# Optimization experiments

Hardware: AMD Instinct MI355X
Metric: run time of the kernel (lower is better)

The kernel has to match this reference:

```python
import jax, jax.numpy as jnp
import numpy as np

D_MODEL = 64
N_HEAD = 4
HEAD_DIM = D_MODEL // N_HEAD  # 16


def setup_inputs() -> dict:
    key = jax.random.key(0)
    ks = jax.random.split(key, 8)
    B, T_dec, T_enc = 16, 1024, 1024
    s = 1.0 / np.sqrt(D_MODEL)
    return {
        "x": jax.random.normal(ks[0], (B, T_dec, D_MODEL), dtype=jnp.float32),
        "encoder_outputs": jax.random.normal(ks[1], (B, T_enc, D_MODEL), dtype=jnp.float32),
        "encoder_outputs_mask": jnp.ones((B, T_enc), dtype=jnp.int32),
        "Wkv": jax.random.normal(ks[2], (D_MODEL, 2 * D_MODEL), dtype=jnp.float32) * s,
        "bkv": jnp.zeros((2 * D_MODEL,), dtype=jnp.float32),
        "Wq": jax.random.normal(ks[3], (D_MODEL, D_MODEL), dtype=jnp.float32) * s,
        "bq": jnp.zeros((D_MODEL,), dtype=jnp.float32),
        "Wproj": jax.random.normal(ks[4], (D_MODEL, D_MODEL), dtype=jnp.float32) * s,
        "bproj": jnp.zeros((D_MODEL,), dtype=jnp.float32),
    }


def reference(x, encoder_outputs, encoder_outputs_mask, Wkv, bkv, Wq, bq, Wproj, bproj):
    B, T_dec, C = x.shape
    T_enc = encoder_outputs.shape[1]
    kv = encoder_outputs @ Wkv + bkv                      # [B, T_enc, 2C]
    k, v = kv[..., :D_MODEL], kv[..., D_MODEL:]          # [B, T_enc, C]
    q = x @ Wq + bq                                      # [B, T_dec, C]
    q = q.reshape(B, T_dec, N_HEAD, HEAD_DIM)
    k = k.reshape(B, T_enc, N_HEAD, HEAD_DIM)
    v = v.reshape(B, T_enc, N_HEAD, HEAD_DIM)
    scale = 1.0 / jnp.sqrt(jnp.asarray(HEAD_DIM, dtype=q.dtype))
    att = jnp.einsum("bqhd,bkhd->bhqk", q, k) * scale    # [B, H, T_dec, T_enc]
    mask = (encoder_outputs_mask == 0)[:, None, None, :]  # [B, 1, 1, T_enc]
    att = jnp.where(mask, jnp.asarray(-jnp.inf, dtype=att.dtype), att)
    att = jax.nn.softmax(att, axis=-1)
    ctx = jnp.einsum("bhqk,bkhd->bqhd", att, v).reshape(B, T_dec, C)
    # dropout is identity at eval time
    return ctx @ Wproj + bproj
```

## Files before the change

### kernel.cpp

```cpp
#include <hip/hip_runtime.h>
#include <hip/hip_bf16.h>
#include <math.h>

#define DM 64
#define NH 4
#define HD 16
#define BATCH 16
#define TSEQ 1024

typedef short bf16x8 __attribute__((ext_vector_type(8)));
typedef short bf16x4 __attribute__((ext_vector_type(4)));
typedef float f32x4  __attribute__((ext_vector_type(4)));
typedef float f32x16 __attribute__((ext_vector_type(16)));
typedef unsigned int u32x4 __attribute__((ext_vector_type(4)));

static __device__ inline short f2bf(float x) {
    __hip_bfloat16 h = __float2bfloat16(x);
    return __builtin_bit_cast(short, h);
}
static __device__ inline float bf2f(short s) {
    __hip_bfloat16 h = __builtin_bit_cast(__hip_bfloat16, s);
    return __bfloat162float(h);
}
static __device__ inline unsigned pkbf(float a, float b) {
    unsigned r;
    asm("v_cvt_pk_bf16_f32 %0, %1, %2" : "=v"(r) : "v"(a), "v"(b));
    return r;
}

__global__ __launch_bounds__(256) void proj_kernel(
    const float* __restrict__ x, const float* __restrict__ enc,
    const float* __restrict__ Wkv, const float* __restrict__ bkv,
    const float* __restrict__ Wq,  const float* __restrict__ bq,
    const int* __restrict__ mask,
    short* __restrict__ qhi, short* __restrict__ qlo,
    short* __restrict__ khi, short* __restrict__ klo,
    short* __restrict__ vtt)
{
    const int t = threadIdx.x;
    const int part = blockIdx.y;
    const int r = blockIdx.x * 256 + t;
    const int b = r >> 10, trow = r & 1023;

    const float* in; const float* W; const float* bias; int cb, ldw;
    if (part < 4)      { in = x;   W = Wq;  ldw = 64;  cb = part*16;          bias = bq;  }
    else if (part < 8) { in = enc; W = Wkv; ldw = 128; cb = (part-4)*16;      bias = bkv; }
    else               { in = enc; W = Wkv; ldw = 128; cb = 64 + (part-8)*16; bias = bkv; }

    __shared__ float wsl[64][16];
    for (int idx = t; idx < 1024; idx += 256)
        wsl[idx >> 4][idx & 15] = W[(idx >> 4)*ldw + cb + (idx & 15)];

    float4 xr[16];
    const float4* inrow = (const float4*)(in + (size_t)r * 64);
    #pragma unroll
    for (int i = 0; i < 16; ++i) xr[i] = inrow[i];
    __syncthreads();

    float acc[16];
    #pragma unroll
    for (int j = 0; j < 16; ++j) acc[j] = bias[cb + j];
    #pragma unroll
    for (int k = 0; k < 64; ++k) {
        const float xv = ((const float*)xr)[k];
        const float4 w0 = ((const float4*)&wsl[k][0])[0];
        const float4 w1 = ((const float4*)&wsl[k][0])[1];
        const float4 w2 = ((const float4*)&wsl[k][0])[2];
        const float4 w3 = ((const float4*)&wsl[k][0])[3];
        acc[0]  += xv*w0.x; acc[1]  += xv*w0.y; acc[2]  += xv*w0.z; acc[3]  += xv*w0.w;
        acc[4]  += xv*w1.x; acc[5]  += xv*w1.y; acc[6]  += xv*w1.z; acc[7]  += xv*w1.w;
        acc[8]  += xv*w2.x; acc[9]  += xv*w2.y; acc[10] += xv*w2.z; acc[11] += xv*w2.w;
        acc[12] += xv*w3.x; acc[13] += xv*w3.y; acc[14] += xv*w3.z; acc[15] += xv*w3.w;
    }

    if (part < 8) {
        const float scale = (part < 4) ? 0.36067376022224085f : 1.0f;
        short* dh = (part < 4) ? qhi : khi;
        short* dl = (part < 4) ? qlo : klo;
        const int h = (part < 4) ? part : (part - 4);
        bf16x8 h0, h1, l0, l1;
        #pragma unroll
        for (int j = 0; j < 16; ++j) {
            float vf = acc[j] * scale;
            short hb = f2bf(vf);
            short lb = f2bf(vf - bf2f(hb));
            if (j < 8) { h0[j] = hb; l0[j] = lb; }
            else       { h1[j-8] = hb; l1[j-8] = lb; }
        }
        size_t off = (((size_t)(b*NH + h))*TSEQ + trow)*HD;
        *(bf16x8*)(dh + off)     = h0;
        *(bf16x8*)(dh + off + 8) = h1;
        *(bf16x8*)(dl + off)     = l0;
        *(bf16x8*)(dl + off + 8) = l1;
    } else {
        const int h = part - 8;
        const float mb = (mask[b*TSEQ + trow] != 0) ? 1.0f : 0.0f;
        short* tile = vtt + ((size_t)(b*NH + h))*32768 + (size_t)(trow >> 5)*1024;
        const int kw = trow & 31;
        #pragma unroll
        for (int j = 0; j < 16; ++j)
            tile[j*32 + kw] = f2bf(acc[j] * mb);
        tile[16*32 + kw] = (mb != 0.0f) ? (short)0x3F80 : (short)0;
    }
}

__global__ __launch_bounds__(512) void attn_kernel(
    const short* __restrict__ qhi, const short* __restrict__ qlo,
    const short* __restrict__ khi, const short* __restrict__ klo,
    const short* __restrict__ vtt,
    const float* __restrict__ Wproj, const float* __restrict__ bproj,
    float* __restrict__ out)
{
    const int tid  = threadIdx.x;
    const int lane = tid & 63;
    const int wid  = __builtin_amdgcn_readfirstlane(tid >> 6);
    const int h  = wid & 3;
    const int ks = wid >> 2;
    const int l31 = lane & 31, half = lane >> 5;

    const int bi  = blockIdx.x;
    const int xcd = bi & 7, u = bi >> 3;
    const int b     = xcd + ((u >> 5) << 3);
    const int qbase = (u & 31) * 32;

    __shared__ float Cbuf[2][32][68];
    __shared__ float Lbuf[2][NH][32];
    __shared__ u32x4 Wl[2][4][2][64];

    #pragma unroll
    for (int it = 0; it < 2; ++it) {
        const int s = tid + it*512;
        const int lane6 = s & 63;
        const int hl  = (s >> 6) & 1;
        const int stp = (s >> 7) & 3;
        const int ctc = s >> 9;
        const int c  = ctc*32 + (lane6 & 31);
        const int kb = stp*16 + (lane6 >> 5)*8;
        u32x4 wv;
        #pragma unroll
        for (int jj = 0; jj < 4; ++jj) {
            const float w0 = Wproj[(kb + 2*jj)*DM + c];
            const float w1 = Wproj[(kb + 2*jj + 1)*DM + c];
            if (hl == 0) {
                wv[jj] = pkbf(w0, w1);
            } else {
                const float h0 = bf2f(f2bf(w0));
                const float h1 = bf2f(f2bf(w1));
                wv[jj] = pkbf(w0 - h0, w1 - h1);
            }
        }
        Wl[ctc][stp][hl][lane6] = wv;
    }
    __syncthreads();

    const size_t qoff = (((size_t)(b*NH + h))*TSEQ + qbase + l31)*HD + half*8;
    const bf16x8 qAh = *(const bf16x8*)(qhi + qoff);
    const bf16x8 qAl = *(const bf16x8*)(qlo + qoff);

    const short* khb = khi + (((size_t)(b*NH + h))*TSEQ + ks*512)*HD;
    const short* klb = klo + (((size_t)(b*NH + h))*TSEQ + ks*512)*HD;
    const short* vtb = vtt + ((size_t)(b*NH + h))*32768 + (size_t)ks*16384;

    f32x16 Cacc;
    #pragma unroll
    for (int i = 0; i < 16; ++i) Cacc[i] = 0.f;

    for (int step = 0; step < 16; ++step) {
        const int ko = step * 32;
        const bf16x8 kBh = *(const bf16x8*)(khb + (size_t)(ko + l31)*HD + half*8);
        const bf16x8 kBl = *(const bf16x8*)(klb + (size_t)(ko + l31)*HD + half*8);
        const short* tile = vtb + (size_t)step * 1024;
        const bf16x8 vB0 = *(const bf16x8*)(tile + l31*32 + half*8);
        const bf16x8 vB1 = *(const bf16x8*)(tile + l31*32 + 16 + half*8);

        f32x16 S;
        #pragma unroll
        for (int i = 0; i < 16; ++i) S[i] = 0.f;
        S = __builtin_amdgcn_mfma_f32_32x32x16_bf16(kBh, qAh, S, 0, 0, 0);
        S = __builtin_amdgcn_mfma_f32_32x32x16_bf16(kBl, qAh, S, 0, 0, 0);
        S = __builtin_amdgcn_mfma_f32_32x32x16_bf16(kBh, qAl, S, 0, 0, 0);

        float p[16];
        #pragma unroll
        for (int i = 0; i < 16; ++i) p[i] = __builtin_amdgcn_exp2f(S[i]);

        unsigned a0 = pkbf(p[0],  p[1]),  b0 = pkbf(p[4],  p[5]);
        unsigned a1 = pkbf(p[2],  p[3]),  b1 = pkbf(p[6],  p[7]);
        unsigned a2 = pkbf(p[8],  p[9]),  b2 = pkbf(p[12], p[13]);
        unsigned a3 = pkbf(p[10], p[11]), b3 = pkbf(p[14], p[15]);
        asm("v_permlane32_swap_b32 %0, %1" : "+v"(a0), "+v"(b0));
        asm("v_permlane32_swap_b32 %0, %1" : "+v"(a1), "+v"(b1));
        asm("v_permlane32_swap_b32 %0, %1" : "+v"(a2), "+v"(b2));
        asm("v_permlane32_swap_b32 %0, %1" : "+v"(a3), "+v"(b3));
        u32x4 P0v; P0v[0] = a0; P0v[1] = a1; P0v[2] = b0; P0v[3] = b1;
        u32x4 P1v; P1v[0] = a2; P1v[1] = a3; P1v[2] = b2; P1v[3] = b3;
        const bf16x8 pA0 = __builtin_bit_cast(bf16x8, P0v);
        const bf16x8 pA1 = __builtin_bit_cast(bf16x8, P1v);

        Cacc = __builtin_amdgcn_mfma_f32_32x32x16_bf16(pA0, vB0, Cacc, 0, 0, 0);
        Cacc = __builtin_amdgcn_mfma_f32_32x32x16_bf16(pA1, vB1, Cacc, 0, 0, 0);
    }

    #pragma unroll
    for (int r = 0; r < 16; ++r) {
        const int row = (r & 3) + 8*(r >> 2) + 4*half;
        if (l31 < 16)        Cbuf[ks][row][h*HD + l31] = Cacc[r];
        else if (l31 == 16)  Lbuf[ks][h][row] = Cacc[r];
    }
    __syncthreads();

    if (wid < 2) {
        const int ct = wid;
        const int t  = l31;
        const int c  = ct*32 + l31;
        f32x16 D;
        const float bp = bproj[c];
        #pragma unroll
        for (int i = 0; i < 16; ++i) D[i] = bp;

        #pragma unroll
        for (int stp = 0; stp < 4; ++stp) {
            const float linv = 1.0f / (Lbuf[0][stp][t] + Lbuf[1][stp][t]);
            const int ib = stp*16 + half*8;
            const float4 x0 = *(const float4*)&Cbuf[0][t][ib];
            const float4 x1 = *(const float4*)&Cbuf[0][t][ib+4];
            const float4 y0 = *(const float4*)&Cbuf[1][t][ib];
            const float4 y1 = *(const float4*)&Cbuf[1][t][ib+4];
            float cv[8];
            cv[0] = (x0.x+y0.x)*linv; cv[1] = (x0.y+y0.y)*linv;
            cv[2] = (x0.z+y0.z)*linv; cv[3] = (x0.w+y0.w)*linv;
            cv[4] = (x1.x+y1.x)*linv; cv[5] = (x1.y+y1.y)*linv;
            cv[6] = (x1.z+y1.z)*linv; cv[7] = (x1.w+y1.w)*linv;
            u32x4 Ahv, Alv;
            #pragma unroll
            for (int jj = 0; jj < 4; ++jj) {
                const unsigned hw = pkbf(cv[2*jj], cv[2*jj+1]);
                const float h0 = bf2f((short)(hw & 0xffff));
                const float h1 = bf2f((short)(hw >> 16));
                Ahv[jj] = hw;
                Alv[jj] = pkbf(cv[2*jj] - h0, cv[2*jj+1] - h1);
            }
            const bf16x8 Ah = __builtin_bit_cast(bf16x8, Ahv);
            const bf16x8 Al = __builtin_bit_cast(bf16x8, Alv);
            const bf16x8 Bh = __builtin_bit_cast(bf16x8, Wl[ct][stp][0][lane]);
            const bf16x8 Bl = __builtin_bit_cast(bf16x8, Wl[ct][stp][1][lane]);
            D = __builtin_amdgcn_mfma_f32_32x32x16_bf16(Ah, Bh, D, 0, 0, 0);
            D = __builtin_amdgcn_mfma_f32_32x32x16_bf16(Ah, Bl, D, 0, 0, 0);
            D = __builtin_amdgcn_mfma_f32_32x32x16_bf16(Al, Bh, D, 0, 0, 0);
        }
        float* orow = out + ((size_t)b*TSEQ + qbase)*DM + c;
        #pragma unroll
        for (int r = 0; r < 16; ++r) {
            const int tr = (r & 3) + 8*(r >> 2) + 4*half;
            orow[(size_t)tr * DM] = D[r];
        }
    }
}

extern "C" void kernel_launch(void* const* d_in, const int* in_sizes, int n_in,
                              void* d_out, int out_size, void* d_ws, size_t ws_size,
                              hipStream_t stream) {
    const float* x     = (const float*)d_in[0];
    const float* enc   = (const float*)d_in[1];
    const int*   mask  = (const int*)  d_in[2];
    const float* Wkv   = (const float*)d_in[3];
    const float* bkv   = (const float*)d_in[4];
    const float* Wq    = (const float*)d_in[5];
    const float* bq    = (const float*)d_in[6];
    const float* Wproj = (const float*)d_in[7];
    const float* bproj = (const float*)d_in[8];
    float* out = (float*)d_out;

    const size_t SZ = (size_t)BATCH*NH*TSEQ*HD;
    short* qhi = (short*)d_ws;
    short* qlo = qhi + SZ;
    short* khi = qlo + SZ;
    short* klo = khi + SZ;
    short* vtt = klo + SZ;

    proj_kernel<<<dim3(64, 12), dim3(256), 0, stream>>>(
        x, enc, Wkv, bkv, Wq, bq, mask, qhi, qlo, khi, klo, vtt);
    attn_kernel<<<dim3(512), dim3(512), 0, stream>>>(
        qhi, qlo, khi, klo, vtt, Wproj, bproj, out);
}
```

Before: 106.5 us.

## Process two 32-row query tiles per block to reuse K/V loads

```diff
diff --git a/kernel.cpp b/kernel.cpp
--- a/kernel.cpp
+++ b/kernel.cpp
@@ -26,6 +26,24 @@
     unsigned r;
     asm("v_cvt_pk_bf16_f32 %0, %1, %2" : "=v"(r) : "v"(a), "v"(b));
     return r;
+}
+
+static __device__ inline void softmax_frags(const f32x16& S, bf16x8& pA0, bf16x8& pA1) {
+    float p[16];
+    #pragma unroll
+    for (int i = 0; i < 16; ++i) p[i] = __builtin_amdgcn_exp2f(S[i]);
+    unsigned a0 = pkbf(p[0],  p[1]),  b0 = pkbf(p[4],  p[5]);
+    unsigned a1 = pkbf(p[2],  p[3]),  b1 = pkbf(p[6],  p[7]);
+    unsigned a2 = pkbf(p[8],  p[9]),  b2 = pkbf(p[12], p[13]);
+    unsigned a3 = pkbf(p[10], p[11]), b3 = pkbf(p[14], p[15]);
+    asm("v_permlane32_swap_b32 %0, %1" : "+v"(a0), "+v"(b0));
+    asm("v_permlane32_swap_b32 %0, %1" : "+v"(a1), "+v"(b1));
+    asm("v_permlane32_swap_b32 %0, %1" : "+v"(a2), "+v"(b2));
+    asm("v_permlane32_swap_b32 %0, %1" : "+v"(a3), "+v"(b3));
+    u32x4 P0v; P0v[0] = a0; P0v[1] = a1; P0v[2] = b0; P0v[3] = b1;
+    u32x4 P1v; P1v[0] = a2; P1v[1] = a3; P1v[2] = b2; P1v[3] = b3;
+    pA0 = __builtin_bit_cast(bf16x8, P0v);
+    pA1 = __builtin_bit_cast(bf16x8, P1v);
 }
 
 __global__ __launch_bounds__(256) void proj_kernel(
@@ -120,11 +138,11 @@
 
     const int bi  = blockIdx.x;
     const int xcd = bi & 7, u = bi >> 3;
-    const int b     = xcd + ((u >> 5) << 3);
-    const int qbase = (u & 31) * 32;
-
-    __shared__ float Cbuf[2][32][68];
-    __shared__ float Lbuf[2][NH][32];
+    const int b     = xcd + ((u >> 4) << 3);
+    const int qbase = (u & 15) * 64;
+
+    __shared__ float Cbuf[2][64][68];
+    __shared__ float Lbuf[2][NH][64];
     __shared__ u32x4 Wl[2][4][2][64];
 
     #pragma unroll
@@ -154,16 +172,18 @@
     __syncthreads();
 
     const size_t qoff = (((size_t)(b*NH + h))*TSEQ + qbase + l31)*HD + half*8;
-    const bf16x8 qAh = *(const bf16x8*)(qhi + qoff);
-    const bf16x8 qAl = *(const bf16x8*)(qlo + qoff);
+    const bf16x8 qAh0 = *(const bf16x8*)(qhi + qoff);
+    const bf16x8 qAl0 = *(const bf16x8*)(qlo + qoff);
+    const bf16x8 qAh1 = *(const bf16x8*)(qhi + qoff + 32*HD);
+    const bf16x8 qAl1 = *(const bf16x8*)(qlo + qoff + 32*HD);
 
     const short* khb = khi + (((size_t)(b*NH + h))*TSEQ + ks*512)*HD;
     const short* klb = klo + (((size_t)(b*NH + h))*TSEQ + ks*512)*HD;
     const short* vtb = vtt + ((size_t)(b*NH + h))*32768 + (size_t)ks*16384;
 
-    f32x16 Cacc;
-    #pragma unroll
-    for (int i = 0; i < 16; ++i) Cacc[i] = 0.f;
+    f32x16 Cacc0, Cacc1;
+    #pragma unroll
+    for (int i = 0; i < 16; ++i) { Cacc0[i] = 0.f; Cacc1[i] = 0.f; }
 
     for (int step = 0; step < 16; ++step) {
         const int ko = step * 32;
@@ -173,45 +193,48 @@
         const bf16x8 vB0 = *(const bf16x8*)(tile + l31*32 + half*8);
         const bf16x8 vB1 = *(const bf16x8*)(tile + l31*32 + 16 + half*8);
 
-        f32x16 S;
-        #pragma unroll
-        for (int i = 0; i < 16; ++i) S[i] = 0.f;
-        S = __builtin_amdgcn_mfma_f32_32x32x16_bf16(kBh, qAh, S, 0, 0, 0);
-        S = __builtin_amdgcn_mfma_f32_32x32x16_bf16(kBl, qAh, S, 0, 0, 0);
-        S = __builtin_amdgcn_mfma_f32_32x32x16_bf16(kBh, qAl, S, 0, 0, 0);
-
-        float p[16];
-        #pragma unroll
-        for (int i = 0; i < 16; ++i) p[i] = __builtin_amdgcn_exp2f(S[i]);
-
-        unsigned a0 = pkbf(p[0],  p[1]),  b0 = pkbf(p[4],  p[5]);
-        unsigned a1 = pkbf(p[2],  p[3]),  b1 = pkbf(p[6],  p[7]);
-        unsigned a2 = pkbf(p[8],  p[9]),  b2 = pkbf(p[12], p[13]);
-        unsigned a3 = pkbf(p[10], p[11]), b3 = pkbf(p[14], p[15]);
-        asm("v_permlane32_swap_b32 %0, %1" : "+v"(a0), "+v"(b0));
-        asm("v_permlane32_swap_b32 %0, %1" : "+v"(a1), "+v"(b1));
-        asm("v_permlane32_swap_b32 %0, %1" : "+v"(a2), "+v"(b2));
-        asm("v_permlane32_swap_b32 %0, %1" : "+v"(a3), "+v"(b3));
-        u32x4 P0v; P0v[0] = a0; P0v[1] = a1; P0v[2] = b0; P0v[3] = b1;
-        u32x4 P1v; P1v[0] = a2; P1v[1] = a3; P1v[2] = b2; P1v[3] = b3;
-        const bf16x8 pA0 = __builtin_bit_cast(bf16x8, P0v);
-        const bf16x8 pA1 = __builtin_bit_cast(bf16x8, P1v);
-
-        Cacc = __builtin_amdgcn_mfma_f32_32x32x16_bf16(pA0, vB0, Cacc, 0, 0, 0);
-        Cacc = __builtin_amdgcn_mfma_f32_32x32x16_bf16(pA1, vB1, Cacc, 0, 0, 0);
+        {
+            f32x16 S;
+            #pragma unroll
+            for (int i = 0; i < 16; ++i) S[i] = 0.f;
+            S = __builtin_amdgcn_mfma_f32_32x32x16_bf16(kBh, qAh0, S, 0, 0, 0);
+            S = __builtin_amdgcn_mfma_f32_32x32x16_bf16(kBl, qAh0, S, 0, 0, 0);
+            S = __builtin_amdgcn_mfma_f32_32x32x16_bf16(kBh, qAl0, S, 0, 0, 0);
+            bf16x8 pA0, pA1;
+            softmax_frags(S, pA0, pA1);
+            Cacc0 = __builtin_amdgcn_mfma_f32_32x32x16_bf16(pA0, vB0, Cacc0, 0, 0, 0);
+            Cacc0 = __builtin_amdgcn_mfma_f32_32x32x16_bf16(pA1, vB1, Cacc0, 0, 0, 0);
+        }
+        {
+            f32x16 S;
+            #pragma unroll
+            for (int i = 0; i < 16; ++i) S[i] = 0.f;
+            S = __builtin_amdgcn_mfma_f32_32x32x16_bf16(kBh, qAh1, S, 0, 0, 0);
+            S = __builtin_amdgcn_mfma_f32_32x32x16_bf16(kBl, qAh1, S, 0, 0, 0);
+            S = __builtin_amdgcn_mfma_f32_32x32x16_bf16(kBh, qAl1, S, 0, 0, 0);
+            bf16x8 pA0, pA1;
+            softmax_frags(S, pA0, pA1);
+            Cacc1 = __builtin_amdgcn_mfma_f32_32x32x16_bf16(pA0, vB0, Cacc1, 0, 0, 0);
+            Cacc1 = __builtin_amdgcn_mfma_f32_32x32x16_bf16(pA1, vB1, Cacc1, 0, 0, 0);
+        }
     }
 
     #pragma unroll
     for (int r = 0; r < 16; ++r) {
         const int row = (r & 3) + 8*(r >> 2) + 4*half;
-        if (l31 < 16)        Cbuf[ks][row][h*HD + l31] = Cacc[r];
-        else if (l31 == 16)  Lbuf[ks][h][row] = Cacc[r];
+        if (l31 < 16) {
+            Cbuf[ks][row][h*HD + l31]      = Cacc0[r];
+            Cbuf[ks][32 + row][h*HD + l31] = Cacc1[r];
+        } else if (l31 == 16) {
+            Lbuf[ks][h][row]      = Cacc0[r];
+            Lbuf[ks][h][32 + row] = Cacc1[r];
+        }
     }
     __syncthreads();
 
-    if (wid < 2) {
-        const int ct = wid;
-        const int t  = l31;
+    if (wid < 4) {
+        const int ct = wid & 1, rt = wid >> 1;
+        const int t  = rt*32 + l31;
         const int c  = ct*32 + l31;
         f32x16 D;
         const float bp = bproj[c];
@@ -248,7 +271,7 @@
             D = __builtin_amdgcn_mfma_f32_32x32x16_bf16(Ah, Bl, D, 0, 0, 0);
             D = __builtin_amdgcn_mfma_f32_32x32x16_bf16(Al, Bh, D, 0, 0, 0);
         }
-        float* orow = out + ((size_t)b*TSEQ + qbase)*DM + c;
+        float* orow = out + ((size_t)b*TSEQ + qbase + rt*32)*DM + c;
         #pragma unroll
         for (int r = 0; r < 16; ++r) {
             const int tr = (r & 3) + 8*(r >> 2) + 4*half;
@@ -280,6 +303,6 @@
 
     proj_kernel<<<dim3(64, 12), dim3(256), 0, stream>>>(
         x, enc, Wkv, bkv, Wq, bq, mask, qhi, qlo, khi, klo, vtt);
-    attn_kernel<<<dim3(512), dim3(512), 0, stream>>>(
+    attn_kernel<<<dim3(256), dim3(512), 0, stream>>>(
         qhi, qlo, khi, klo, vtt, Wproj, bproj, out);
 }
```

New measurement: 105.4 us. About the same (-1.1%).
